# Performance work log

Hardware: AMD Instinct MI355X
Metric: run time of the kernel (lower is better)

Reference implementation:

```python
import jax, jax.numpy as jnp
import numpy as np

B, PRIOR, FRAMES, POSE, DMODEL, CHUNK = 256, 60, 240, 768, 768, 10
PRED = FRAMES - PRIOR  # 180
EPS = 1e-5
SCALE = 0.02


def _lin(x, w, b):
    # torch nn.Linear: y = x @ W.T + b, W is [out, in]
    return x @ w.T + b


def setup_inputs() -> dict:
    key = jax.random.key(0)
    ks = jax.random.split(key, 32)
    W = lambda k, o, i: jax.random.normal(k, (o, i), jnp.float32) * SCALE
    V = lambda k, o: jax.random.normal(k, (o,), jnp.float32) * SCALE
    return {
        "x": jax.random.normal(ks[0], (B, PRIOR, POSE), jnp.float32),
        # pred_conv: Conv1d(PRIOR->PRED,k=3,p=1) + BN, Conv1d(PRED->PRED,k=3,p=1) + BN
        "conv1_w": jax.random.normal(ks[1], (PRED, PRIOR, 3), jnp.float32) * SCALE,
        "conv1_b": V(ks[2], PRED),
        "bn1_g": jnp.ones((PRED,), jnp.float32),
        "bn1_b": jnp.zeros((PRED,), jnp.float32),
        "bn1_m": jnp.zeros((PRED,), jnp.float32),
        "bn1_v": jnp.ones((PRED,), jnp.float32),
        "conv2_w": jax.random.normal(ks[3], (PRED, PRED, 3), jnp.float32) * SCALE,
        "conv2_b": V(ks[4], PRED),
        "bn2_g": jnp.ones((PRED,), jnp.float32),
        "bn2_b": jnp.zeros((PRED,), jnp.float32),
        "bn2_m": jnp.zeros((PRED,), jnp.float32),
        "bn2_v": jnp.ones((PRED,), jnp.float32),
        # spatial_chunk_encoder: Linear(CHUNK*POSE -> POSE), Linear(POSE -> POSE)
        "sp_w1": W(ks[5], POSE, CHUNK * POSE), "sp_b1": V(ks[6], POSE),
        "sp_w2": W(ks[7], POSE, POSE), "sp_b2": V(ks[8], POSE),
        # temporal_chunk_encoder: Linear(CHUNK*POSE -> POSE), Linear(POSE -> POSE)
        "tmc_w1": W(ks[9], POSE, CHUNK * POSE), "tmc_b1": V(ks[10], POSE),
        "tmc_w2": W(ks[11], POSE, POSE), "tmc_b2": V(ks[12], POSE),
        # temporal_memory_encoder: Linear(CHUNK*POSE -> CHUNK), Linear(CHUNK -> CHUNK)
        "tmm_w1": W(ks[13], CHUNK, CHUNK * POSE), "tmm_b1": V(ks[14], CHUNK),
        "tmm_w2": W(ks[15], CHUNK, CHUNK), "tmm_b2": V(ks[16], CHUNK),
        # post_header: Linear(POSE -> DMODEL), Linear(DMODEL -> DMODEL)
        "post_w1": W(ks[17], DMODEL, POSE), "post_b1": V(ks[18], DMODEL),
        "post_w2": W(ks[19], DMODEL, DMODEL), "post_b2": V(ks[20], DMODEL),
    }


def reference(x, conv1_w, conv1_b, bn1_g, bn1_b, bn1_m, bn1_v,
              conv2_w, conv2_b, bn2_g, bn2_b, bn2_m, bn2_v,
              sp_w1, sp_b1, sp_w2, sp_b2,
              tmc_w1, tmc_b1, tmc_w2, tmc_b2,
              tmm_w1, tmm_b1, tmm_w2, tmm_b2,
              post_w1, post_b1, post_w2, post_b2):
    Bsz = x.shape[0]

    def conv1d(y, w, b):
        # channels = frames, conv over pose_dim axis, kernel=3, pad=1
        return jax.lax.conv_general_dilated(
            y, w, window_strides=(1,), padding=((1, 1),),
            dimension_numbers=("NCH", "OIH", "NCH")) + b[None, :, None]

    def bn_eval(y, g, b, m, v):
        # BatchNorm1d over channel dim (eval mode, running stats)
        inv = jax.lax.rsqrt(v + EPS)
        return (y - m[None, :, None]) * (inv * g)[None, :, None] + b[None, :, None]

    # pred_conv
    p = bn_eval(jax.nn.relu(conv1d(x, conv1_w, conv1_b)), bn1_g, bn1_b, bn1_m, bn1_v)
    p = bn_eval(jax.nn.relu(conv1d(p, conv2_w, conv2_b)), bn2_g, bn2_b, bn2_m, bn2_v)

    # last CHUNK prior frames, flattened: [B, CHUNK*POSE]
    tail = x[:, PRIOR - CHUNK:, :].reshape(Bsz, -1)

    # --- SP_Memory_Net_v1 (vectorized over the original per-(b,c) loop) ---
    mem = _lin(_lin(tail, sp_w1, sp_b1), sp_w2, sp_b2)            # [B, POSE]
    score = jnp.einsum("bd,bcd->bc", mem, p[:, :CHUNK])           # [B, CHUNK]
    sig = jax.nn.sigmoid(score)[:, :, None]
    chunk_sp = sig * p[:, :CHUNK] + (1.0 - sig) * mem[:, None, :]
    p = jnp.concatenate([chunk_sp, p[:, CHUNK:]], axis=1)

    # --- TM_Memory_Net ---
    mem2 = _lin(_lin(tail, tmc_w1, tmc_b1), tmc_w2, tmc_b2)       # [B, POSE]
    penc = _lin(_lin(p[:, :CHUNK].reshape(Bsz, -1), tmm_w1, tmm_b1), tmm_w2, tmm_b2)  # [B, CHUNK]
    score2 = mem2 @ (mem2.T @ penc)                               # [B, CHUNK]
    soft = jax.nn.softmax(score2, axis=1)
    chunk_tm = p[:, :CHUNK] * (1.0 + soft[:, :, None])
    p = jnp.concatenate([chunk_tm, p[:, CHUNK:]], axis=1)

    # cat prior + predicted frames, then post_header MLP
    out = jnp.concatenate([x, p], axis=1)                          # [B, FRAMES, POSE]
    out = _lin(_lin(out, post_w1, post_b1), post_w2, post_b2)      # [B, FRAMES, DMODEL]
    return out
```

## Files before the change

kernel.cpp:

```cpp
#include <hip/hip_runtime.h>
#include <hip/hip_bf16.h>


using bf16 = __hip_bfloat16;
typedef __attribute__((ext_vector_type(8))) short short8;
typedef __attribute__((ext_vector_type(4))) short s16x4;
typedef __attribute__((ext_vector_type(4))) float f32x4;

#define LDK 40
#define SENT 0xFFFFFFFFu
#define SK_SLICES 24
#define SK_KLEN 320

__device__ __forceinline__ void gld16(const void* g, void* l) {
  __builtin_amdgcn_global_load_lds(
      (const __attribute__((address_space(1))) unsigned int*)g,
      (__attribute__((address_space(3))) unsigned int*)l, 16, 0, 0);
}

struct CvtArgs {
  const void* src[29];
  unsigned hi[29];
  unsigned lo[29];
  unsigned f32[29];
  unsigned n[29];
};

__global__ void detect_k(const unsigned* __restrict__ g, unsigned* __restrict__ flag) {
  if (threadIdx.x == 0) flag[0] = (g[0] == 0x3F803F80u) ? 1u : 0u;
}

__global__ __launch_bounds__(256) void cvt_all(CvtArgs a, char* __restrict__ base,
                                               const unsigned* __restrict__ flag) {
  const bool isbf = (flag[0] != 0u);
  const unsigned e0 = (blockIdx.x * 256u + threadIdx.x) * 4u;
#pragma unroll 1
  for (int i = 0; i < 29; i++) {
    const unsigned n = a.n[i];
    if (e0 >= n) continue;
    bf16* hi = (bf16*)(base + a.hi[i]);
    bf16* lo = (a.lo[i] != SENT) ? (bf16*)(base + a.lo[i]) : nullptr;
    float* fc = (a.f32[i] != SENT) ? (float*)(base + a.f32[i]) : nullptr;
#pragma unroll
    for (int j = 0; j < 4; j++) {
      unsigned e = e0 + j;
      if (e >= n) break;
      float v = isbf ? __bfloat162float(((const bf16*)a.src[i])[e])
                     : ((const float*)a.src[i])[e];
      bf16 h = __float2bfloat16(v);
      hi[e] = h;
      if (lo) lo[e] = __float2bfloat16(v - __bfloat162float(h));
      if (fc) fc[e] = v;
    }
  }
}

__global__ __launch_bounds__(256) void fold_w(
    const float* __restrict__ w1, const float* __restrict__ b1,
    const float* __restrict__ g1, const float* __restrict__ be1,
    const float* __restrict__ m1, const float* __restrict__ v1,
    const float* __restrict__ w2, const float* __restrict__ b2,
    const float* __restrict__ g2, const float* __restrict__ be2,
    const float* __restrict__ m2, const float* __restrict__ v2,
    bf16* __restrict__ Wf1h, bf16* __restrict__ Wf1l,
    bf16* __restrict__ Wf2h, bf16* __restrict__ Wf2l,
    float* __restrict__ bia1, float* __restrict__ s1, float* __restrict__ c1,
    float* __restrict__ bia2, float* __restrict__ s2, float* __restrict__ c2,
    const float* __restrict__ W2p, const float* __restrict__ b1p,
    const float* __restrict__ b2p, float* __restrict__ bfold) {
  int g = blockIdx.x * 256 + threadIdx.x;
  if (g < 192 * 192) {
    int o = g / 192, j = g - o * 192;
    int kk = j >> 6, i = j & 63;
    float v = 0.f;
    if (o < 180 && i < 60) v = w1[(o * 60 + i) * 3 + kk];
    bf16 h = __float2bfloat16(v);
    Wf1h[g] = h;
    Wf1l[g] = __float2bfloat16(v - __bfloat162float(h));
  }
  if (g < 192 * 576) {
    int o = g / 576, j = g - o * 576;
    int kk = j / 192, i = j - kk * 192;
    float v = 0.f;
    if (o < 180 && i < 180) v = w2[(o * 180 + i) * 3 + kk];
    bf16 h = __float2bfloat16(v);
    Wf2h[g] = h;
    Wf2l[g] = __float2bfloat16(v - __bfloat162float(h));
  }
  if (g < 192) {
    if (g < 180) {
      float inv1 = rsqrtf(v1[g] + 1e-5f);
      float sv1 = inv1 * g1[g];
      s1[g] = sv1; c1[g] = be1[g] - m1[g] * sv1; bia1[g] = b1[g];
      float inv2 = rsqrtf(v2[g] + 1e-5f);
      float sv2 = inv2 * g2[g];
      s2[g] = sv2; c2[g] = be2[g] - m2[g] * sv2; bia2[g] = b2[g];
    } else {
      s1[g] = 0.f; c1[g] = 0.f; bia1[g] = 0.f;
      s2[g] = 0.f; c2[g] = 0.f; bia2[g] = 0.f;
    }
  }
  if (g < 768) {
    float s = b2p[g];
    const float* wr = W2p + (size_t)g * 768;
#pragma unroll 4
    for (int d = 0; d < 768; d += 4) {
      f32x4 w4 = *reinterpret_cast<const f32x4*>(wr + d);
      s += b1p[d] * w4[0] + b1p[d + 1] * w4[1] + b1p[d + 2] * w4[2] + b1p[d + 3] * w4[3];
    }
    bfold[g] = s;
  }
}

__global__ __launch_bounds__(256) void transpose_x2(const bf16* __restrict__ xh,
                                                    const bf16* __restrict__ xl,
                                                    bf16* __restrict__ xTh,
                                                    bf16* __restrict__ xTl) {
  __shared__ bf16 t1[64][65];
  __shared__ bf16 t2[64][65];
  const int b = blockIdx.y;
  const int t0 = blockIdx.x * 64;
  const int r = threadIdx.x >> 6;
  const int c = threadIdx.x & 63;
  for (int ii = r; ii < 64; ii += 4) {
    bf16 v1 = __float2bfloat16(0.f), v2 = v1;
    if (ii < 60) {
      v1 = xh[((size_t)b * 60 + ii) * 768 + t0 + c];
      v2 = xl[((size_t)b * 60 + ii) * 768 + t0 + c];
    }
    t1[ii][c] = v1;
    t2[ii][c] = v2;
  }
  __syncthreads();
  for (int tt = r; tt < 64; tt += 4) {
    xTh[((size_t)b * 768 + t0 + tt) * 64 + c] = t1[c][tt];
    xTl[((size_t)b * 768 + t0 + tt) * 64 + c] = t2[c][tt];
  }
}

__global__ __launch_bounds__(256) void transpose_hl(const float* __restrict__ src,
                                                    bf16* __restrict__ th,
                                                    bf16* __restrict__ tl) {
  __shared__ float tile[64][65];
  const int r0 = blockIdx.x * 64;
  const int c0 = blockIdx.y * 64;
  const int r = threadIdx.x >> 6;
  const int c = threadIdx.x & 63;
  for (int rr = r; rr < 64; rr += 4)
    tile[rr][c] = src[(size_t)(r0 + rr) * 768 + c0 + c];
  __syncthreads();
  for (int rr = r; rr < 64; rr += 4) {
    const float v = tile[c][rr];
    bf16 h = __float2bfloat16(v);
    th[(size_t)(c0 + rr) * 768 + r0 + c] = h;
    tl[(size_t)(c0 + rr) * 768 + r0 + c] = __float2bfloat16(v - __bfloat162float(h));
  }
}

template <int SEG, bool TRIP, bool P2C, int EPI>
__global__ __launch_bounds__(256, 2) void conv_k(
    const bf16* __restrict__ A, const bf16* __restrict__ A2,
    const bf16* __restrict__ W, const bf16* __restrict__ W2,
    const float* __restrict__ biasf, const float* __restrict__ bns,
    const float* __restrict__ bnc, void* __restrict__ O1,
    void* __restrict__ O2, int cb0) {
  constexpr int LDA2 = 40;
  constexpr int KW = 3 * SEG;
  constexpr int STG = (TRIP ? 2 : 1) * 130 * LDA2;
  constexpr int TRN = (EPI == 2) ? 4 * 64 * 72 : 0;
  constexpr int LSZ = STG > TRN ? STG : TRN;
  __shared__ short lds[LSZ];
  short* Ah = lds;
  short* Al = lds + 130 * LDA2;

  const int tid = threadIdx.x;
  const int lane = tid & 63;
  const int wave = tid >> 6;
  const int quad = lane >> 4;
  const int l16 = lane & 15;
  const int mtile = blockIdx.x * 128;
  const int t0 = mtile % 768;
  const int bb = mtile / 768;
  const int cb = cb0 + blockIdx.y * 128;
  const int mwave = (wave & 1) * 64;
  const int nwave = (wave >> 1) * 64;

  f32x4 acc[4][4];
#pragma unroll
  for (int i = 0; i < 4; i++)
#pragma unroll
    for (int j = 0; j < 4; j++) acc[i][j] = (f32x4){0.f, 0.f, 0.f, 0.f};

  const short8 z8 = {0, 0, 0, 0, 0, 0, 0, 0};
  for (int ci = 0; ci < SEG; ci += 32) {
#pragma unroll
    for (int l = 0; l < 3; l++) {
      const int idx = tid + l * 256;
      if (idx < 520) {
        const int row = idx >> 2;
        const int cc = (idx & 3) * 8;
        const int tl = t0 + row - 1;
        short8 v = z8, v2 = z8;
        if ((unsigned)tl < 768u) {
          const size_t src = (size_t)(mtile + row - 1) * SEG + ci + cc;
          v = *reinterpret_cast<const short8*>(A + src);
          if constexpr (TRIP) v2 = *reinterpret_cast<const short8*>(A2 + src);
        }
        *reinterpret_cast<short8*>(&Ah[row * LDA2 + cc]) = v;
        if constexpr (TRIP) *reinterpret_cast<short8*>(&Al[row * LDA2 + cc]) = v2;
      }
    }
    __syncthreads();
#pragma unroll
    for (int kk = 0; kk < 3; kk++) {
      short8 bh[4], bl[4];
#pragma unroll
      for (int ni = 0; ni < 4; ni++) {
        const int o = cb + nwave + ni * 16 + l16;
        if (o < 192) {
          const size_t ws = (size_t)o * KW + kk * SEG + ci + quad * 8;
          bh[ni] = *reinterpret_cast<const short8*>(W + ws);
          if constexpr (TRIP) bl[ni] = *reinterpret_cast<const short8*>(W2 + ws);
        } else {
          bh[ni] = z8;
          if constexpr (TRIP) bl[ni] = z8;
        }
      }
#pragma unroll
      for (int mi = 0; mi < 4; mi++) {
        const int ar = (mwave + mi * 16 + l16 + kk) * LDA2 + quad * 8;
        const short8 afh = *reinterpret_cast<const short8*>(&Ah[ar]);
#pragma unroll
        for (int ni = 0; ni < 4; ni++)
          acc[mi][ni] = __builtin_amdgcn_mfma_f32_16x16x32_bf16(afh, bh[ni], acc[mi][ni], 0, 0, 0);
        if constexpr (TRIP) {
          const short8 afl = *reinterpret_cast<const short8*>(&Al[ar]);
#pragma unroll
          for (int ni = 0; ni < 4; ni++) {
            acc[mi][ni] = __builtin_amdgcn_mfma_f32_16x16x32_bf16(afh, bl[ni], acc[mi][ni], 0, 0, 0);
            acc[mi][ni] = __builtin_amdgcn_mfma_f32_16x16x32_bf16(afl, bh[ni], acc[mi][ni], 0, 0, 0);
          }
        }
      }
    }
    __syncthreads();
  }

  if constexpr (EPI == 1) {
#pragma unroll
    for (int mi = 0; mi < 4; mi++)
#pragma unroll
      for (int ni = 0; ni < 4; ni++) {
        const int col = cb + nwave + ni * 16 + l16;
        if (col < 192) {
          const float bv = biasf[col], sv = bns[col], cv = bnc[col];
#pragma unroll
          for (int r = 0; r < 4; r++) {
            const int row = mtile + mwave + mi * 16 + quad * 4 + r;
            float z = fmaxf(acc[mi][ni][r] + bv, 0.f) * sv + cv;
            bf16 h = __float2bfloat16(z);
            ((bf16*)O1)[(size_t)row * 192 + col] = h;
            ((bf16*)O2)[(size_t)row * 192 + col] =
                __float2bfloat16(z - __bfloat162float(h));
          }
        }
      }
  } else {
    if constexpr (P2C) {
#pragma unroll
      for (int mi = 0; mi < 4; mi++)
#pragma unroll
        for (int ni = 0; ni < 4; ni++) {
          const int col = cb + nwave + ni * 16 + l16;
          if (col < 10) {
            const float bv = biasf[col], sv = bns[col], cv = bnc[col];
#pragma unroll
            for (int r = 0; r < 4; r++) {
              const int tloc = t0 + mwave + mi * 16 + quad * 4 + r;
              float z = fmaxf(acc[mi][ni][r] + bv, 0.f) * sv + cv;
              ((float*)O2)[((size_t)bb * 10 + col) * 768 + tloc] = z;
            }
          }
        }
    }
    short* tt = lds + wave * (64 * 72);
#pragma unroll
    for (int ni = 0; ni < 4; ni++) {
      const int col = cb + nwave + ni * 16 + l16;
      const int cx = col < 192 ? col : 0;
      const float bv = biasf[cx], sv = bns[cx], cv = bnc[cx];
#pragma unroll
      for (int mi = 0; mi < 4; mi++) {
        s16x4 pk;
#pragma unroll
        for (int r = 0; r < 4; r++) {
          float z = fmaxf(acc[mi][ni][r] + bv, 0.f) * sv + cv;
          bf16 h = __float2bfloat16(z);
          short sb;
          __builtin_memcpy(&sb, &h, 2);
          pk[r] = sb;
        }
        *reinterpret_cast<s16x4*>(&tt[(ni * 16 + l16) * 72 + mi * 16 + quad * 4]) = pk;
      }
    }
    __syncthreads();
#pragma unroll
    for (int fi = 0; fi < 8; fi++) {
      const int fl = fi * 8 + (lane >> 3);
      const int tch = (lane & 7) * 8;
      const short8 v = *reinterpret_cast<const short8*>(&tt[fl * 72 + tch]);
      const int fg = cb + nwave + fl;
      if (fg < 180)
        *reinterpret_cast<short8*>((bf16*)O1 +
            ((size_t)bb * 180 + fg) * 768 + t0 + mwave + tch) = v;
    }
  }
}

template <int AMODE, int EPI, bool TRIPLE, bool DUALOUT>
__global__ __launch_bounds__(256, 2) void gemm_k(
    const bf16* __restrict__ A, const bf16* __restrict__ A2,
    const bf16* __restrict__ W, const bf16* __restrict__ W2,
    const float* __restrict__ biasf, void* __restrict__ Cv,
    void* __restrict__ Cv2, const unsigned* __restrict__ oflag,
    int N, int K, int lda, int ldc) {
  __shared__ __align__(16) short As[128 * 32];
  __shared__ __align__(16) short Bs[128 * 32];
  __shared__ __align__(16) short As2[TRIPLE ? 128 * 32 : 8];
  __shared__ __align__(16) short Bs2[TRIPLE ? 128 * 32 : 8];
  const int tid = threadIdx.x;
  const int lane = tid & 63;
  const int wave = tid >> 6;
  const int quad = lane >> 4;
  const int l16 = lane & 15;
  const int mtile = blockIdx.x * 128;
  const int ntile = blockIdx.y * 128;
  const int mwave = (wave & 1) * 64;
  const int nwave = (wave >> 1) * 64;

  f32x4 acc[4][4];
#pragma unroll
  for (int i = 0; i < 4; i++)
#pragma unroll
    for (int j = 0; j < 4; j++) acc[i][j] = (f32x4){0.f, 0.f, 0.f, 0.f};

  for (int k0 = 0; k0 < K; k0 += 32) {
#pragma unroll
    for (int l = 0; l < 2; l++) {
      const int e = tid + l * 256;
      const int row = e >> 2;
      const int gk = k0 + (((e & 3) ^ ((e >> 3) & 3)) << 3);
      const bf16* ga;
      if constexpr (AMODE == 0) {
        ga = A + (size_t)(mtile + row) * lda + gk;
      } else {
        const int gr = mtile + row;
        const int b = gr / 240;
        const int f = gr - b * 240;
        ga = (f < 60) ? (A + ((size_t)b * 60 + f) * 768 + gk)
                      : (A2 + ((size_t)b * 180 + (f - 60)) * 768 + gk);
      }
      gld16(ga, &As[l * 2048 + wave * 512]);
      gld16(W + (size_t)(ntile + row) * K + gk, &Bs[l * 2048 + wave * 512]);
      if constexpr (TRIPLE) {
        gld16(A2 + (size_t)(mtile + row) * lda + gk, &As2[l * 2048 + wave * 512]);
        gld16(W2 + (size_t)(ntile + row) * K + gk, &Bs2[l * 2048 + wave * 512]);
      }
    }
    __syncthreads();
    short8 af[4], bfr[4];
#pragma unroll
    for (int mi = 0; mi < 4; mi++) {
      const int r = mwave + mi * 16 + l16;
      af[mi] = *reinterpret_cast<const short8*>(&As[r * 32 + ((quad ^ ((r >> 1) & 3)) << 3)]);
    }
#pragma unroll
    for (int ni = 0; ni < 4; ni++) {
      const int r = nwave + ni * 16 + l16;
      bfr[ni] = *reinterpret_cast<const short8*>(&Bs[r * 32 + ((quad ^ ((r >> 1) & 3)) << 3)]);
    }
#pragma unroll
    for (int mi = 0; mi < 4; mi++)
#pragma unroll
      for (int ni = 0; ni < 4; ni++)
        acc[mi][ni] = __builtin_amdgcn_mfma_f32_16x16x32_bf16(af[mi], bfr[ni], acc[mi][ni], 0, 0, 0);
    if constexpr (TRIPLE) {
      short8 afl[4], bfl[4];
#pragma unroll
      for (int mi = 0; mi < 4; mi++) {
        const int r = mwave + mi * 16 + l16;
        afl[mi] = *reinterpret_cast<const short8*>(&As2[r * 32 + ((quad ^ ((r >> 1) & 3)) << 3)]);
      }
#pragma unroll
      for (int ni = 0; ni < 4; ni++) {
        const int r = nwave + ni * 16 + l16;
        bfl[ni] = *reinterpret_cast<const short8*>(&Bs2[r * 32 + ((quad ^ ((r >> 1) & 3)) << 3)]);
      }
#pragma unroll
      for (int mi = 0; mi < 4; mi++)
#pragma unroll
        for (int ni = 0; ni < 4; ni++) {
          acc[mi][ni] = __builtin_amdgcn_mfma_f32_16x16x32_bf16(af[mi], bfl[ni], acc[mi][ni], 0, 0, 0);
          acc[mi][ni] = __builtin_amdgcn_mfma_f32_16x16x32_bf16(afl[mi], bfr[ni], acc[mi][ni], 0, 0, 0);
        }
    }
    __syncthreads();
  }

  const unsigned outbf = DUALOUT ? oflag[0] : 1u;
#pragma unroll
  for (int mi = 0; mi < 4; mi++) {
#pragma unroll
    for (int ni = 0; ni < 4; ni++) {
      const int col = ntile + nwave + ni * 16 + l16;
#pragma unroll
      for (int r = 0; r < 4; r++) {
        const int row = mtile + mwave + mi * 16 + quad * 4 + r;
        float v = acc[mi][ni][r];
        if constexpr (EPI == 4) {
          bf16 h = __float2bfloat16(v);
          ((bf16*)Cv)[(size_t)row * ldc + col] = h;
          ((bf16*)Cv2)[(size_t)row * ldc + col] =
              __float2bfloat16(v - __bfloat162float(h));
        } else {
          v += biasf[col];
          if constexpr (DUALOUT) {
            if (outbf) ((bf16*)Cv)[(size_t)row * ldc + col] = __float2bfloat16(v);
            else       ((float*)Cv)[(size_t)row * ldc + col] = v;
          } else {
            ((float*)Cv)[(size_t)row * ldc + col] = v;
          }
        }
      }
    }
  }
  (void)N;
}

__global__ __launch_bounds__(256, 2) void mlp_sk(
    const bf16* __restrict__ Ah, const bf16* __restrict__ Al,
    const bf16* __restrict__ Wh0, const bf16* __restrict__ Wl0,
    const bf16* __restrict__ Wh1, const bf16* __restrict__ Wl1,
    float* __restrict__ part) {
  __shared__ short As[128 * LDK];
  __shared__ short Bs[128 * LDK];
  __shared__ short As2[128 * LDK];
  __shared__ short Bs2[128 * LDK];
  const int tid = threadIdx.x;
  const int lane = tid & 63;
  const int wave = tid >> 6;
  const int quad = lane >> 4;
  const int l16 = lane & 15;
  const int mtile = blockIdx.x * 128;
  const int ntile = blockIdx.y * 128;
  const int net = blockIdx.z / SK_SLICES;
  const int slice = blockIdx.z - net * SK_SLICES;
  const int kbase = slice * SK_KLEN;
  const bf16* __restrict__ Wh = net ? Wh1 : Wh0;
  const bf16* __restrict__ Wl = net ? Wl1 : Wl0;
  const int mwave = (wave & 1) * 64;
  const int nwave = (wave >> 1) * 64;

  f32x4 acc[4][4];
#pragma unroll
  for (int i = 0; i < 4; i++)
#pragma unroll
    for (int j = 0; j < 4; j++) acc[i][j] = (f32x4){0.f, 0.f, 0.f, 0.f};

  for (int ks = 0; ks < SK_KLEN; ks += 32) {
#pragma unroll
    for (int l = 0; l < 2; l++) {
      const int e = tid + l * 256;
      const int row = e >> 2;
      const int kcol = (e & 3) * 8;
      const int gk = kbase + ks + kcol;
      *reinterpret_cast<short8*>(&As[row * LDK + kcol]) =
          *reinterpret_cast<const short8*>(Ah + (size_t)(mtile + row) * 46080 + gk);
      *reinterpret_cast<short8*>(&As2[row * LDK + kcol]) =
          *reinterpret_cast<const short8*>(Al + (size_t)(mtile + row) * 46080 + gk);
      *reinterpret_cast<short8*>(&Bs[row * LDK + kcol]) =
          *reinterpret_cast<const short8*>(Wh + (size_t)(ntile + row) * 7680 + gk);
      *reinterpret_cast<short8*>(&Bs2[row * LDK + kcol]) =
          *reinterpret_cast<const short8*>(Wl + (size_t)(ntile + row) * 7680 + gk);
    }
    __syncthreads();
    short8 af[4], bfr[4], afl[4], bfl[4];
#pragma unroll
    for (int mi = 0; mi < 4; mi++) {
      af[mi] = *reinterpret_cast<const short8*>(&As[(mwave + mi * 16 + l16) * LDK + quad * 8]);
      afl[mi] = *reinterpret_cast<const short8*>(&As2[(mwave + mi * 16 + l16) * LDK + quad * 8]);
    }
#pragma unroll
    for (int ni = 0; ni < 4; ni++) {
      bfr[ni] = *reinterpret_cast<const short8*>(&Bs[(nwave + ni * 16 + l16) * LDK + quad * 8]);
      bfl[ni] = *reinterpret_cast<const short8*>(&Bs2[(nwave + ni * 16 + l16) * LDK + quad * 8]);
    }
#pragma unroll
    for (int mi = 0; mi < 4; mi++)
#pragma unroll
      for (int ni = 0; ni < 4; ni++) {
        acc[mi][ni] = __builtin_amdgcn_mfma_f32_16x16x32_bf16(af[mi], bfr[ni], acc[mi][ni], 0, 0, 0);
        acc[mi][ni] = __builtin_amdgcn_mfma_f32_16x16x32_bf16(af[mi], bfl[ni], acc[mi][ni], 0, 0, 0);
        acc[mi][ni] = __builtin_amdgcn_mfma_f32_16x16x32_bf16(afl[mi], bfr[ni], acc[mi][ni], 0, 0, 0);
      }
    __syncthreads();
  }

  float* __restrict__ dst = part + ((size_t)net * SK_SLICES + slice) * 196608;
#pragma unroll
  for (int mi = 0; mi < 4; mi++) {
#pragma unroll
    for (int ni = 0; ni < 4; ni++) {
      const int col = ntile + nwave + ni * 16 + l16;
#pragma unroll
      for (int r = 0; r < 4; r++) {
        const int row = mtile + mwave + mi * 16 + quad * 4 + r;
        dst[(size_t)row * 768 + col] = acc[mi][ni][r];
      }
    }
  }
}

__global__ __launch_bounds__(256) void mlp_tail(
    const float* __restrict__ part, const float* __restrict__ bsp,
    const float* __restrict__ btm, const float* __restrict__ Wsp,
    const float* __restrict__ b2sp, const float* __restrict__ Wtm,
    const float* __restrict__ b2tm, float* __restrict__ mem,
    float* __restrict__ mem2) {
  const int net = blockIdx.x >> 8;
  const int b = blockIdx.x & 255;
  const int tid = threadIdx.x;
  __shared__ float As[768];
#pragma unroll
  for (int j = 0; j < 3; j++) {
    const int col = tid + j * 256;
    const float* p = part + (size_t)net * SK_SLICES * 196608 + (size_t)b * 768 + col;
    float s = 0.f;
#pragma unroll
    for (int i = 0; i < SK_SLICES; i++) s += p[(size_t)i * 196608];
    As[col] = s + (net ? btm[col] : bsp[col]);
  }
  __syncthreads();
  const float* W = net ? Wtm : Wsp;
  const float* b2 = net ? b2tm : b2sp;
  float* out = net ? mem2 : mem;
#pragma unroll 1
  for (int j = 0; j < 3; j++) {
    const int o = tid + j * 256;
    float s = b2[o];
    const float* wr = W + (size_t)o * 768;
#pragma unroll 4
    for (int k = 0; k < 768; k += 4) {
      f32x4 w4 = *reinterpret_cast<const f32x4*>(wr + k);
      s += As[k] * w4[0] + As[k + 1] * w4[1] + As[k + 2] * w4[2] + As[k + 3] * w4[3];
    }
    out[(size_t)b * 768 + o] = s;
  }
}

__global__ __launch_bounds__(256) void sp_tm(const float* __restrict__ mem,
                                             float* __restrict__ p2c,
                                             const float* __restrict__ w1,
                                             const float* __restrict__ b1,
                                             float* __restrict__ th) {
  const int b = blockIdx.x;
  const int tid = threadIdx.x;
  __shared__ float row[7680];
  __shared__ float red[4];
  __shared__ float sval;
  for (int i = tid; i < 7680; i += 256) row[i] = p2c[(size_t)b * 7680 + i];
  float mv[3];
#pragma unroll
  for (int j = 0; j < 3; j++) mv[j] = mem[(size_t)b * 768 + tid + j * 256];
  __syncthreads();
  for (int c = 0; c < 10; c++) {
    const int base = c * 768;
    float pv[3];
    float part = 0.f;
#pragma unroll
    for (int j = 0; j < 3; j++) {
      pv[j] = row[base + tid + j * 256];
      part += pv[j] * mv[j];
    }
#pragma unroll
    for (int off = 32; off; off >>= 1) part += __shfl_down(part, off);
    if ((tid & 63) == 0) red[tid >> 6] = part;
    __syncthreads();
    if (tid == 0) sval = 1.f / (1.f + expf(-(red[0] + red[1] + red[2] + red[3])));
    __syncthreads();
    const float sg = sval;
#pragma unroll
    for (int j = 0; j < 3; j++)
      row[base + tid + j * 256] = sg * pv[j] + (1.f - sg) * mv[j];
    __syncthreads();
  }
  for (int i = tid; i < 7680; i += 256) p2c[(size_t)b * 7680 + i] = row[i];
  float part[10] = {0.f, 0.f, 0.f, 0.f, 0.f, 0.f, 0.f, 0.f, 0.f, 0.f};
#pragma unroll 1
  for (int k = tid; k < 7680; k += 256) {
    const float v = row[k];
#pragma unroll
    for (int c = 0; c < 10; c++) part[c] += v * w1[(size_t)c * 7680 + k];
  }
  __shared__ float red10[10][4];
#pragma unroll
  for (int c = 0; c < 10; c++) {
    float p = part[c];
#pragma unroll
    for (int off = 32; off; off >>= 1) p += __shfl_down(p, off);
    if ((tid & 63) == 0) red10[c][tid >> 6] = p;
  }
  __syncthreads();
  if (tid < 10)
    th[b * 10 + tid] = red10[tid][0] + red10[tid][1] + red10[tid][2] + red10[tid][3] + b1[tid];
}

__global__ __launch_bounds__(256) void tm_G2(const float* __restrict__ th,
                                             const float* __restrict__ w2,
                                             const float* __restrict__ b2,
                                             const float* __restrict__ mem2,
                                             float* __restrict__ G) {
  __shared__ float penc[256 * 10];
  const int tid = threadIdx.x;
  {
    float h[10];
#pragma unroll
    for (int j = 0; j < 10; j++) h[j] = th[tid * 10 + j];
#pragma unroll
    for (int c = 0; c < 10; c++) {
      float s = b2[c];
#pragma unroll
      for (int j = 0; j < 10; j++) s += h[j] * w2[c * 10 + j];
      penc[tid * 10 + c] = s;
    }
  }
  __syncthreads();
  const int idx = blockIdx.x * 256 + tid;
  if (idx >= 7680) return;
  const int d = idx / 10, c = idx - d * 10;
  float s = 0.f;
  for (int b = 0; b < 256; b++) s += mem2[(size_t)b * 768 + d] * penc[b * 10 + c];
  G[idx] = s;
}

__global__ __launch_bounds__(256) void tm_scale(const float* __restrict__ mem2,
                                                const float* __restrict__ G,
                                                const float* __restrict__ p2c,
                                                bf16* __restrict__ p2) {
  const int b = blockIdx.x;
  const int tid = threadIdx.x;
  float part[10] = {0.f, 0.f, 0.f, 0.f, 0.f, 0.f, 0.f, 0.f, 0.f, 0.f};
#pragma unroll
  for (int j = 0; j < 3; j++) {
    const int d = tid + j * 256;
    const float v = mem2[(size_t)b * 768 + d];
#pragma unroll
    for (int c = 0; c < 10; c++) part[c] += v * G[d * 10 + c];
  }
  __shared__ float red[10][4];
  __shared__ float soft[10];
#pragma unroll
  for (int c = 0; c < 10; c++) {
    float p = part[c];
#pragma unroll
    for (int off = 32; off; off >>= 1) p += __shfl_down(p, off);
    if ((tid & 63) == 0) red[c][tid >> 6] = p;
  }
  __syncthreads();
  if (tid == 0) {
    float sc[10], mx = -1e30f;
#pragma unroll
    for (int c = 0; c < 10; c++) {
      sc[c] = red[c][0] + red[c][1] + red[c][2] + red[c][3];
      mx = fmaxf(mx, sc[c]);
    }
    float sum = 0.f;
#pragma unroll
    for (int c = 0; c < 10; c++) { sc[c] = expf(sc[c] - mx); sum += sc[c]; }
#pragma unroll
    for (int c = 0; c < 10; c++) soft[c] = sc[c] / sum;
  }
  __syncthreads();
  for (int idx = tid; idx < 7680; idx += 256) {
    const int c = idx / 768;
    const int t = idx - c * 768;
    const float val = p2c[(size_t)b * 7680 + idx] * (1.f + soft[c]);
    p2[((size_t)b * 180 + c) * 768 + t] = __float2bfloat16(val);
  }
}

extern "C" void kernel_launch(void* const* d_in, const int* in_sizes, int n_in,
                              void* d_out, int out_size, void* d_ws, size_t ws_size,
                              hipStream_t stream) {
  char* base = (char*)d_ws;
  size_t off = 0;
  auto take = [&](size_t bytes) {
    size_t o = off;
    off += (bytes + 255) & ~(size_t)255;
    return o;
  };
  size_t hi[29], lo[29], f32c[29];
  for (int i = 0; i < 29; i++) { lo[i] = (size_t)SENT; f32c[i] = (size_t)SENT; }
  for (int i = 0; i < 29 && i < n_in; i++) hi[i] = take((size_t)in_sizes[i] * 2);
  lo[0] = take((size_t)in_sizes[0] * 2);
  lo[13] = take((size_t)in_sizes[13] * 2);
  lo[17] = take((size_t)in_sizes[17] * 2);
  lo[27] = take((size_t)in_sizes[27] * 2);
  const int f32set[] = {1, 2, 3, 4, 5, 6, 7, 8, 9, 10, 11, 12,
                        14, 15, 16, 18, 19, 20, 21, 22, 23, 24,
                        25, 26, 27, 28};
  for (int i : f32set) f32c[i] = take((size_t)in_sizes[i] * 4);

  const size_t flagOff = take(16);
  const size_t wf1hOff = take(192 * 192 * 2), wf1lOff = take(192 * 192 * 2);
  const size_t wf2hOff = take(192 * 576 * 2), wf2lOff = take(192 * 576 * 2);
  const size_t bia1Off = take(192 * 4), s1Off = take(192 * 4), c1Off = take(192 * 4);
  const size_t bia2Off = take(192 * 4), s2Off = take(192 * 4), c2Off = take(192 * 4);
  const size_t w1thOff = take(768 * 768 * 2), w1tlOff = take(768 * 768 * 2);
  const size_t wfhOff = take(768 * 768 * 2), wflOff = take(768 * 768 * 2);
  const size_t bfoldOff = take(768 * 4);
  const size_t memOff = take(256 * 768 * 4);
  const size_t mem2Off = take(256 * 768 * 4);
  const size_t thOff = take(256 * 10 * 4);
  const size_t gOff = take(7680 * 4);
  const size_t xThOff = take((size_t)256 * 768 * 64 * 2);
  const size_t xTlOff = take((size_t)256 * 768 * 64 * 2);
  const size_t p1hOff = take((size_t)196608 * 192 * 2);
  const size_t p1lOff = take((size_t)196608 * 192 * 2);
  const size_t p2Off = take((size_t)256 * 180 * 768 * 2);
  const size_t p2cOff = take((size_t)256 * 7680 * 4);
  const size_t partOff = p1lOff;
  (void)ws_size; (void)out_size;

  auto B16 = [&](size_t o) { return (bf16*)(base + o); };
  auto F32 = [&](size_t o) { return (float*)(base + o); };
  unsigned* flag = (unsigned*)(base + flagOff);

  detect_k<<<1, 64, 0, stream>>>((const unsigned*)d_in[3], flag);

  CvtArgs ca;
  for (int i = 0; i < 29; i++) {
    ca.src[i] = d_in[i];
    ca.hi[i] = (unsigned)hi[i];
    ca.lo[i] = (unsigned)lo[i];
    ca.f32[i] = (unsigned)f32c[i];
    ca.n[i] = (unsigned)in_sizes[i];
  }
  cvt_all<<<11520, 256, 0, stream>>>(ca, base, flag);

  fold_w<<<432, 256, 0, stream>>>(
      F32(f32c[1]), F32(f32c[2]), F32(f32c[3]), F32(f32c[4]), F32(f32c[5]), F32(f32c[6]),
      F32(f32c[7]), F32(f32c[8]), F32(f32c[9]), F32(f32c[10]), F32(f32c[11]), F32(f32c[12]),
      B16(wf1hOff), B16(wf1lOff), B16(wf2hOff), B16(wf2lOff),
      F32(bia1Off), F32(s1Off), F32(c1Off), F32(bia2Off), F32(s2Off), F32(c2Off),
      F32(f32c[27]), F32(f32c[26]), F32(f32c[28]), F32(bfoldOff));

  transpose_hl<<<dim3(12, 12), 256, 0, stream>>>(F32(f32c[25]), B16(w1thOff), B16(w1tlOff));
  gemm_k<0, 4, true, false><<<dim3(6, 6), 256, 0, stream>>>(
      B16(hi[27]), B16(lo[27]), B16(w1thOff), B16(w1tlOff), nullptr,
      base + wfhOff, base + wflOff, nullptr, 768, 768, 768, 768);

  transpose_x2<<<dim3(12, 256), 256, 0, stream>>>(B16(hi[0]), B16(lo[0]),
                                                  B16(xThOff), B16(xTlOff));

  conv_k<64, true, false, 1><<<dim3(1536, 2), 256, 0, stream>>>(
      B16(xThOff), B16(xTlOff), B16(wf1hOff), B16(wf1lOff),
      F32(bia1Off), F32(s1Off), F32(c1Off), base + p1hOff, base + p1lOff, 0);
  conv_k<192, true, true, 2><<<dim3(1536, 1), 256, 0, stream>>>(
      B16(p1hOff), B16(p1lOff), B16(wf2hOff), B16(wf2lOff),
      F32(bia2Off), F32(s2Off), F32(c2Off), base + p2Off, base + p2cOff, 0);
  conv_k<192, false, false, 2><<<dim3(1536, 1), 256, 0, stream>>>(
      B16(p1hOff), nullptr, B16(wf2hOff), nullptr,
      F32(bia2Off), F32(s2Off), F32(c2Off), base + p2Off, nullptr, 128);

  mlp_sk<<<dim3(2, 6, 48), 256, 0, stream>>>(
      B16(hi[0]) + 38400, B16(lo[0]) + 38400,
      B16(hi[13]), B16(lo[13]), B16(hi[17]), B16(lo[17]), F32(partOff));
  mlp_tail<<<512, 256, 0, stream>>>(F32(partOff), F32(f32c[14]), F32(f32c[18]),
                                    F32(f32c[15]), F32(f32c[16]),
                                    F32(f32c[19]), F32(f32c[20]),
                                    F32(memOff), F32(mem2Off));

  sp_tm<<<256, 256, 0, stream>>>(F32(memOff), F32(p2cOff), F32(f32c[21]),
                                 F32(f32c[22]), F32(thOff));
  tm_G2<<<30, 256, 0, stream>>>(F32(thOff), F32(f32c[23]), F32(f32c[24]),
                                F32(mem2Off), F32(gOff));
  tm_scale<<<256, 256, 0, stream>>>(F32(mem2Off), F32(gOff), F32(p2cOff), B16(p2Off));

  gemm_k<2, 0, false, true><<<dim3(480, 6), 256, 0, stream>>>(
      B16(hi[0]), B16(p2Off), B16(wfhOff), nullptr, F32(bfoldOff),
      d_out, nullptr, flag, 768, 768, 0, 768);
}
```

Baseline: 1.072 ms.

## Move second memory-encoder linear layer onto split-bf16 MFMA GEMM with split-K

Replaces the scalar fp32 mlp_tail kernel, which reduced the split-K partials and then ran a 768x768 matvec per batch row, with three kernels. The first reduces the partials and splits the activations into bf16 hi/lo. The second is an MFMA GEMM using three bf16 products (hi*hi, hi*lo, lo*hi) with a 6-way K split. The third reduces those partials and adds the bias. The aim is to put the second linear layer on matrix cores instead of a per-thread fp32 dot loop. The cost is two extra launches, extra workspace traffic, and slightly different rounding from the hi/lo bf16 emulation of fp32.

Measured after the change: 945.8 us. 1.13x faster.

```diff
diff --git a/kernel.cpp b/kernel.cpp
--- a/kernel.cpp
+++ b/kernel.cpp
@@ -521,41 +521,125 @@
   }
 }
 
-__global__ __launch_bounds__(256) void mlp_tail(
+__global__ __launch_bounds__(256) void mlp_red(
     const float* __restrict__ part, const float* __restrict__ bsp,
-    const float* __restrict__ btm, const float* __restrict__ Wsp,
-    const float* __restrict__ b2sp, const float* __restrict__ Wtm,
+    const float* __restrict__ btm, bf16* __restrict__ a2h,
+    bf16* __restrict__ a2l) {
+  const int idx = blockIdx.x * 256 + threadIdx.x;
+  const int net = (idx >= 196608) ? 1 : 0;
+  const int e = idx - net * 196608;
+  const float* p = part + (size_t)net * SK_SLICES * 196608 + e;
+  float s = 0.f;
+#pragma unroll
+  for (int i = 0; i < SK_SLICES; i++) s += p[(size_t)i * 196608];
+  const int col = e - (e / 768) * 768;
+  s += net ? btm[col] : bsp[col];
+  bf16 h = __float2bfloat16(s);
+  a2h[idx] = h;
+  a2l[idx] = __float2bfloat16(s - __bfloat162float(h));
+}
+
+__global__ __launch_bounds__(256, 2) void mlp_l2(
+    const bf16* __restrict__ a2h, const bf16* __restrict__ a2l,
+    const bf16* __restrict__ Wh0, const bf16* __restrict__ Wl0,
+    const bf16* __restrict__ Wh1, const bf16* __restrict__ Wl1,
+    float* __restrict__ part2) {
+  __shared__ short As[128 * LDK];
+  __shared__ short Bs[128 * LDK];
+  __shared__ short As2[128 * LDK];
+  __shared__ short Bs2[128 * LDK];
+  const int tid = threadIdx.x;
+  const int lane = tid & 63;
+  const int wave = tid >> 6;
+  const int quad = lane >> 4;
+  const int l16 = lane & 15;
+  const int mtile = blockIdx.x * 128;
+  const int ntile = blockIdx.y * 128;
+  const int net = blockIdx.z / 6;
+  const int slice = blockIdx.z - net * 6;
+  const int kbase = slice * 128;
+  const bf16* __restrict__ Ah = a2h + (size_t)net * 196608;
+  const bf16* __restrict__ Al = a2l + (size_t)net * 196608;
+  const bf16* __restrict__ Wh = net ? Wh1 : Wh0;
+  const bf16* __restrict__ Wl = net ? Wl1 : Wl0;
+  const int mwave = (wave & 1) * 64;
+  const int nwave = (wave >> 1) * 64;
+
+  f32x4 acc[4][4];
+#pragma unroll
+  for (int i = 0; i < 4; i++)
+#pragma unroll
+    for (int j = 0; j < 4; j++) acc[i][j] = (f32x4){0.f, 0.f, 0.f, 0.f};
+
+  for (int ks = 0; ks < 128; ks += 32) {
+#pragma unroll
+    for (int l = 0; l < 2; l++) {
+      const int e = tid + l * 256;
+      const int row = e >> 2;
+      const int kcol = (e & 3) * 8;
+      const int gk = kbase + ks + kcol;
+      *reinterpret_cast<short8*>(&As[row * LDK + kcol]) =
+          *reinterpret_cast<const short8*>(Ah + (size_t)(mtile + row) * 768 + gk);
+      *reinterpret_cast<short8*>(&As2[row * LDK + kcol]) =
+          *reinterpret_cast<const short8*>(Al + (size_t)(mtile + row) * 768 + gk);
+      *reinterpret_cast<short8*>(&Bs[row * LDK + kcol]) =
+          *reinterpret_cast<const short8*>(Wh + (size_t)(ntile + row) * 768 + gk);
+      *reinterpret_cast<short8*>(&Bs2[row * LDK + kcol]) =
+          *reinterpret_cast<const short8*>(Wl + (size_t)(ntile + row) * 768 + gk);
+    }
+    __syncthreads();
+    short8 af[4], bfr[4], afl[4], bfl[4];
+#pragma unroll
+    for (int mi = 0; mi < 4; mi++) {
+      af[mi] = *reinterpret_cast<const short8*>(&As[(mwave + mi * 16 + l16) * LDK + quad * 8]);
+      afl[mi] = *reinterpret_cast<const short8*>(&As2[(mwave + mi * 16 + l16) * LDK + quad * 8]);
+    }
+#pragma unroll
+    for (int ni = 0; ni < 4; ni++) {
+      bfr[ni] = *reinterpret_cast<const short8*>(&Bs[(nwave + ni * 16 + l16) * LDK + quad * 8]);
+      bfl[ni] = *reinterpret_cast<const short8*>(&Bs2[(nwave + ni * 16 + l16) * LDK + quad * 8]);
+    }
+#pragma unroll
+    for (int mi = 0; mi < 4; mi++)
+#pragma unroll
+      for (int ni = 0; ni < 4; ni++) {
+        acc[mi][ni] = __builtin_amdgcn_mfma_f32_16x16x32_bf16(af[mi], bfr[ni], acc[mi][ni], 0, 0, 0);
+        acc[mi][ni] = __builtin_amdgcn_mfma_f32_16x16x32_bf16(af[mi], bfl[ni], acc[mi][ni], 0, 0, 0);
+        acc[mi][ni] = __builtin_amdgcn_mfma_f32_16x16x32_bf16(afl[mi], bfr[ni], acc[mi][ni], 0, 0, 0);
+      }
+    __syncthreads();
+  }
+
+  float* __restrict__ dst = part2 + ((size_t)net * 6 + slice) * 196608;
+#pragma unroll
+  for (int mi = 0; mi < 4; mi++) {
+#pragma unroll
+    for (int ni = 0; ni < 4; ni++) {
+      const int col = ntile + nwave + ni * 16 + l16;
+#pragma unroll
+      for (int r = 0; r < 4; r++) {
+        const int row = mtile + mwave + mi * 16 + quad * 4 + r;
+        dst[(size_t)row * 768 + col] = acc[mi][ni][r];
+      }
+    }
+  }
+}
+
+__global__ __launch_bounds__(256) void mlp_red2(
+    const float* __restrict__ part2, const float* __restrict__ b2sp,
     const float* __restrict__ b2tm, float* __restrict__ mem,
     float* __restrict__ mem2) {
-  const int net = blockIdx.x >> 8;
-  const int b = blockIdx.x & 255;
-  const int tid = threadIdx.x;
-  __shared__ float As[768];
-#pragma unroll
-  for (int j = 0; j < 3; j++) {
-    const int col = tid + j * 256;
-    const float* p = part + (size_t)net * SK_SLICES * 196608 + (size_t)b * 768 + col;
-    float s = 0.f;
-#pragma unroll
-    for (int i = 0; i < SK_SLICES; i++) s += p[(size_t)i * 196608];
-    As[col] = s + (net ? btm[col] : bsp[col]);
-  }
-  __syncthreads();
-  const float* W = net ? Wtm : Wsp;
-  const float* b2 = net ? b2tm : b2sp;
-  float* out = net ? mem2 : mem;
-#pragma unroll 1
-  for (int j = 0; j < 3; j++) {
-    const int o = tid + j * 256;
-    float s = b2[o];
-    const float* wr = W + (size_t)o * 768;
-#pragma unroll 4
-    for (int k = 0; k < 768; k += 4) {
-      f32x4 w4 = *reinterpret_cast<const f32x4*>(wr + k);
-      s += As[k] * w4[0] + As[k + 1] * w4[1] + As[k + 2] * w4[2] + As[k + 3] * w4[3];
-    }
-    out[(size_t)b * 768 + o] = s;
-  }
+  const int idx = blockIdx.x * 256 + threadIdx.x;
+  const int net = (idx >= 196608) ? 1 : 0;
+  const int e = idx - net * 196608;
+  const float* p = part2 + (size_t)net * 6 * 196608 + e;
+  float s = 0.f;
+#pragma unroll
+  for (int i = 0; i < 6; i++) s += p[(size_t)i * 196608];
+  const int col = e - (e / 768) * 768;
+  s += net ? b2tm[col] : b2sp[col];
+  if (net) mem2[e] = s;
+  else     mem[e] = s;
 }
 
 __global__ __launch_bounds__(256) void sp_tm(const float* __restrict__ mem,
@@ -704,7 +788,9 @@
   for (int i = 0; i < 29 && i < n_in; i++) hi[i] = take((size_t)in_sizes[i] * 2);
   lo[0] = take((size_t)in_sizes[0] * 2);
   lo[13] = take((size_t)in_sizes[13] * 2);
+  lo[15] = take((size_t)in_sizes[15] * 2);
   lo[17] = take((size_t)in_sizes[17] * 2);
+  lo[19] = take((size_t)in_sizes[19] * 2);
   lo[27] = take((size_t)in_sizes[27] * 2);
   const int f32set[] = {1, 2, 3, 4, 5, 6, 7, 8, 9, 10, 11, 12,
                         14, 15, 16, 18, 19, 20, 21, 22, 23, 24,
@@ -723,6 +809,9 @@
   const size_t mem2Off = take(256 * 768 * 4);
   const size_t thOff = take(256 * 10 * 4);
   const size_t gOff = take(7680 * 4);
+  const size_t a2hOff = take((size_t)2 * 196608 * 2);
+  const size_t a2lOff = take((size_t)2 * 196608 * 2);
+  const size_t part2Off = take((size_t)2 * 6 * 196608 * 4);
   const size_t xThOff = take((size_t)256 * 768 * 64 * 2);
   const size_t xTlOff = take((size_t)256 * 768 * 64 * 2);
   const size_t p1hOff = take((size_t)196608 * 192 * 2);
@@ -776,10 +865,13 @@
   mlp_sk<<<dim3(2, 6, 48), 256, 0, stream>>>(
       B16(hi[0]) + 38400, B16(lo[0]) + 38400,
       B16(hi[13]), B16(lo[13]), B16(hi[17]), B16(lo[17]), F32(partOff));
-  mlp_tail<<<512, 256, 0, stream>>>(F32(partOff), F32(f32c[14]), F32(f32c[18]),
-                                    F32(f32c[15]), F32(f32c[16]),
-                                    F32(f32c[19]), F32(f32c[20]),
-                                    F32(memOff), F32(mem2Off));
+  mlp_red<<<1536, 256, 0, stream>>>(F32(partOff), F32(f32c[14]), F32(f32c[18]),
+                                    B16(a2hOff), B16(a2lOff));
+  mlp_l2<<<dim3(2, 6, 12), 256, 0, stream>>>(
+      B16(a2hOff), B16(a2lOff), B16(hi[15]), B16(lo[15]),
+      B16(hi[19]), B16(lo[19]), F32(part2Off));
+  mlp_red2<<<1536, 256, 0, stream>>>(F32(part2Off), F32(f32c[16]), F32(f32c[20]),
+                                     F32(memOff), F32(mem2Off));
 
   sp_tm<<<256, 256, 0, stream>>>(F32(memOff), F32(p2cOff), F32(f32c[21]),
                                  F32(f32c[22]), F32(thOff));
```
